# Kernel optimization log

Measured on AMD Instinct MI355X. Metric: run time of the kernel, lower is better.

Reference implementation:

```python
import jax, jax.numpy as jnp
import numpy as np

EMB = 64          # emb_size
LG = 64           # lg_msg_dim
NDB = 16          # num_dist_basis
NCB = 16          # num_cos_basis
NCLS = 40
NLAYERS = 2
NJK = NLAYERS + 2  # jumping-knowledge sequence length
HID = (NJK * EMB) // 2  # PyG JK-LSTM hidden size = 128


def setup_inputs() -> dict:
    key = jax.random.key(0)
    ks = jax.random.split(key, 24)
    N, Eg, Elg, F = 50000, 800000, 800000, 128
    s = 0.05
    inp = {
        "x": jax.random.normal(ks[0], (N, F), jnp.float32),
        "edge_index_g": jax.random.randint(ks[1], (2, Eg), 0, N, jnp.int32),
        "edge_attr_g": jax.random.uniform(ks[2], (Eg, NDB), jnp.float32),
        "edge_index_lg": jax.random.randint(ks[3], (2, Elg), 0, Eg, jnp.int32),
        "edge_attr_lg": jax.random.uniform(ks[4], (Elg, NCB), jnp.float32),
        # parameters (nn.Linear convention: W is [out, in])
        "W_feat": jax.random.normal(ks[5], (EMB, F), jnp.float32) * s,
        "W_msg": jax.random.normal(ks[6], (LG, 2 * EMB + NDB), jnp.float32) * s,
        "W_lg2g": jax.random.normal(ks[7], (EMB, LG), jnp.float32) * s,
        "b_lg2g": jax.random.normal(ks[8], (EMB,), jnp.float32) * s,
        "W_msg_layers": jax.random.normal(ks[9], (NLAYERS, LG, 2 * LG + NCB), jnp.float32) * s,
        # bidirectional LSTM params (PyTorch gate order i,f,g,o)
        "Wih_f": jax.random.normal(ks[10], (4 * HID, EMB), jnp.float32) * s,
        "Whh_f": jax.random.normal(ks[11], (4 * HID, HID), jnp.float32) * s,
        "bih_f": jax.random.normal(ks[12], (4 * HID,), jnp.float32) * s,
        "bhh_f": jax.random.normal(ks[13], (4 * HID,), jnp.float32) * s,
        "Wih_b": jax.random.normal(ks[14], (4 * HID, EMB), jnp.float32) * s,
        "Whh_b": jax.random.normal(ks[15], (4 * HID, HID), jnp.float32) * s,
        "bih_b": jax.random.normal(ks[16], (4 * HID,), jnp.float32) * s,
        "bhh_b": jax.random.normal(ks[17], (4 * HID,), jnp.float32) * s,
        "W_att": jax.random.normal(ks[18], (1, 2 * HID), jnp.float32) * s,
        "b_att": jax.random.normal(ks[19], (1,), jnp.float32) * s,
        "W_out": jax.random.normal(ks[20], (NCLS, EMB), jnp.float32) * s,
    }
    return inp


def _lstm(x_seq, Wih, Whh, bih, bhh, reverse):
    # x_seq: [N, L, C] -> hs: [N, L, H]
    N = x_seq.shape[0]
    H = Whh.shape[1]
    b = bih + bhh

    def step(carry, x_t):
        h, c = carry
        gates = x_t @ Wih.T + h @ Whh.T + b
        i, f, g, o = jnp.split(gates, 4, axis=-1)
        c = jax.nn.sigmoid(f) * c + jax.nn.sigmoid(i) * jnp.tanh(g)
        h = jax.nn.sigmoid(o) * jnp.tanh(c)
        return (h, c), h

    xs = jnp.swapaxes(x_seq, 0, 1)  # [L, N, C]
    init = (jnp.zeros((N, H), x_seq.dtype), jnp.zeros((N, H), x_seq.dtype))
    _, hs = jax.lax.scan(step, init, xs, reverse=reverse)
    return jnp.swapaxes(hs, 0, 1)


def reference(x, edge_index_g, edge_attr_g, edge_index_lg, edge_attr_lg,
              W_feat, W_msg, W_lg2g, b_lg2g, W_msg_layers,
              Wih_f, Whh_f, bih_f, bhh_f, Wih_b, Whh_b, bih_b, bhh_b,
              W_att, b_att, W_out):
    N = x.shape[0]
    Eg = edge_attr_g.shape[0]
    seg = jax.ops.segment_sum

    # node embedding (eval mode: dropout is identity)
    node_emb = jax.nn.relu(x @ W_feat.T)  # [N, EMB]

    # initial linegraph node features: gather endpoints -> concat -> linear -> relu
    m1 = node_emb[edge_index_g[0]]  # [Eg, EMB]
    m2 = node_emb[edge_index_g[1]]
    msg_emb = jax.nn.relu(jnp.concatenate([m1, m2, edge_attr_g], -1) @ W_msg.T)  # [Eg, LG]

    node_embs = [node_emb]
    msg_red = msg_emb @ W_lg2g.T + b_lg2g
    node_embs.append(seg(msg_red, edge_index_g[1], num_segments=N))

    # message-passing layers on the linegraph
    for l in range(W_msg_layers.shape[0]):
        s = msg_emb[edge_index_lg[0]]
        d = msg_emb[edge_index_lg[1]]
        m = jax.nn.relu(jnp.concatenate([s, d, edge_attr_lg], -1) @ W_msg_layers[l].T)
        msg_emb = seg(m, edge_index_lg[1], num_segments=Eg)  # scatter_add over linegraph
        incoming = seg(msg_emb, edge_index_g[1], num_segments=N)
        node_embs.append(incoming @ W_lg2g.T + b_lg2g)

    # JumpingKnowledge ('lstm'): bidirectional LSTM -> attention -> weighted sum
    x_jk = jnp.stack(node_embs, axis=1)  # [N, NJK, EMB]
    h_f = _lstm(x_jk, Wih_f, Whh_f, bih_f, bhh_f, reverse=False)
    h_b = _lstm(x_jk, Wih_b, Whh_b, bih_b, bhh_b, reverse=True)
    h = jnp.concatenate([h_f, h_b], -1)  # [N, NJK, 2*HID]
    alpha = jax.nn.softmax((h @ W_att.T + b_att)[..., 0], axis=-1)  # [N, NJK]
    final_emb = jnp.sum(x_jk * alpha[..., None], axis=1)  # [N, EMB]

    out = final_emb @ W_out.T
    return jax.nn.log_softmax(out, axis=-1)
```

## Files before the change

### kernel.cpp

```cpp
#include <hip/hip_runtime.h>

typedef unsigned short u16;
typedef unsigned int u32;
typedef __attribute__((ext_vector_type(8))) short bf16x8;
typedef __attribute__((ext_vector_type(4))) float f32x4;

#define MFMA(a, b, c) __builtin_amdgcn_mfma_f32_16x16x32_bf16(a, b, c, 0, 0, 0)

__device__ __forceinline__ u16 f2bf(float x) {
    union { float f; u32 u; } v; v.f = x;
    u32 r = (v.u + 0x7FFFu + ((v.u >> 16) & 1u)) >> 16;
    return (u16)r;
}
__device__ __forceinline__ float bf2f(u16 b) {
    union { u32 u; float f; } v; v.u = ((u32)b) << 16;
    return v.f;
}
__device__ __forceinline__ void casAddPair(u32* w, float lo, float hi) {
    u32 old = *w, assumed;
    do {
        assumed = old;
        u32 des = (u32)f2bf(bf2f((u16)(assumed & 0xFFFFu)) + lo) |
                  ((u32)f2bf(bf2f((u16)(assumed >> 16)) + hi) << 16);
        if (des == assumed) break;
        old = atomicCAS(w, assumed, des);
    } while (old != assumed);
}

__global__ __launch_bounds__(256) void prep_w(
    const float* __restrict__ Whh_f, const float* __restrict__ Whh_b,
    const float* __restrict__ Wih_f, const float* __restrict__ Wih_b,
    const float* __restrict__ bih_f, const float* __restrict__ bhh_f,
    const float* __restrict__ bih_b, const float* __restrict__ bhh_b,
    const float* __restrict__ W_feat, const float* __restrict__ W_msg,
    const float* __restrict__ W_msg_l, const float* __restrict__ W_lg2g,
    u16* __restrict__ WhhB, u16* __restrict__ WihB, float* __restrict__ BS,
    u16* __restrict__ WfeatB, u16* __restrict__ WmsgB,
    u16* __restrict__ WmsgLB, u16* __restrict__ Wlg2gB)
{
    const float L2E = 1.4426950408889634f;
    int i = blockIdx.x * 256 + threadIdx.x;
    if (i < 131072) {
        int d = i >> 16, r = i & 65535;
        float s = (((r >> 14) & 3) == 2) ? 2.f * L2E : L2E;
        WhhB[i] = f2bf(s * (d ? Whh_b[r] : Whh_f[r]));
    } else if (i < 196608) {
        int i2 = i - 131072; int d = i2 >> 15, r = i2 & 32767;
        float s = (((r >> 13) & 3) == 2) ? 2.f * L2E : L2E;
        WihB[i2] = f2bf(s * (d ? Wih_b[r] : Wih_f[r]));
    } else if (i < 197632) {
        int i3 = i - 196608; int d = i3 >> 9, g = i3 & 511;
        float s = (((g >> 7) & 3) == 2) ? 2.f * L2E : L2E;
        BS[i3] = s * (d ? (bih_b[g] + bhh_b[g]) : (bih_f[g] + bhh_f[g]));
    } else if (i < 205824) {
        int j = i - 197632; WfeatB[j] = f2bf(W_feat[j]);
    } else if (i < 215040) {
        int j = i - 205824; WmsgB[j] = f2bf(W_msg[j]);
    } else if (i < 233472) {
        int j = i - 215040; WmsgLB[j] = f2bf(W_msg_l[j]);
    } else if (i < 237568) {
        int j = i - 233472; Wlg2gB[j] = f2bf(W_lg2g[j]);
    }
}

__global__ __launch_bounds__(256) void count_kernel(const int* __restrict__ dst,
                                                    u32* __restrict__ cnt, long E)
{
    long i = (long)blockIdx.x * 256 + threadIdx.x;
    if (i < E) atomicAdd(&cnt[dst[i]], 1u);
}

__global__ __launch_bounds__(256) void scan1(const u32* __restrict__ a,
                                             u32* __restrict__ part, int n)
{
    __shared__ u32 ts[256];
    int b = blockIdx.x, t = threadIdx.x;
    long i0 = (long)b * 1024 + t * 4;
    u32 s = 0;
#pragma unroll
    for (int k = 0; k < 4; ++k) { long i = i0 + k; if (i < n) s += a[i]; }
    ts[t] = s; __syncthreads();
    for (int off = 1; off < 256; off <<= 1) {
        u32 x = (t >= off) ? ts[t - off] : 0u;
        __syncthreads(); ts[t] += x; __syncthreads();
    }
    if (t == 255) part[b] = ts[255];
}

__global__ __launch_bounds__(1024) void scan2(u32* __restrict__ part, int nb,
                                              u32* __restrict__ total_out)
{
    __shared__ u32 ts[1024];
    int t = threadIdx.x;
    u32 v = (t < nb) ? part[t] : 0u;
    ts[t] = v; __syncthreads();
    for (int off = 1; off < 1024; off <<= 1) {
        u32 x = (t >= off) ? ts[t - off] : 0u;
        __syncthreads(); ts[t] += x; __syncthreads();
    }
    if (t < nb) part[t] = ts[t] - v;
    if (t == 1023 && total_out) *total_out = ts[1023];
}

__global__ __launch_bounds__(256) void scan3(u32* __restrict__ a,
                                             const u32* __restrict__ part, int n)
{
    __shared__ u32 ts[256];
    int b = blockIdx.x, t = threadIdx.x;
    long i0 = (long)b * 1024 + t * 4;
    u32 v[4]; u32 s = 0;
#pragma unroll
    for (int k = 0; k < 4; ++k) { long i = i0 + k; v[k] = (i < n) ? a[i] : 0u; s += v[k]; }
    ts[t] = s; __syncthreads();
    for (int off = 1; off < 256; off <<= 1) {
        u32 x = (t >= off) ? ts[t - off] : 0u;
        __syncthreads(); ts[t] += x; __syncthreads();
    }
    u32 run = part[b] + ts[t] - s;
#pragma unroll
    for (int k = 0; k < 4; ++k) {
        long i = i0 + k;
        if (i < n) { u32 x = v[k]; a[i] = run; run += x; }
    }
}

__global__ __launch_bounds__(256) void fill_kernel(const int* __restrict__ dst,
                                                   u32* __restrict__ off,
                                                   int* __restrict__ list, long E)
{
    long i = (long)blockIdx.x * 256 + threadIdx.x;
    if (i < E) {
        u32 pos = atomicAdd(&off[dst[i]], 1u);
        list[pos] = (int)i;
    }
}

__global__ __launch_bounds__(256) void zero_fill(const u32* __restrict__ offc,
                                                 u16* __restrict__ outb, long NB)
{
    long idx = (long)blockIdx.x * 256 + threadIdx.x;
    long n = idx >> 3; int q = (int)(idx & 7);
    if (n >= NB) return;
    u32 s = n ? offc[n - 1] : 0u;
    u32 e = offc[n];
    bool need = (s == e) || ((s >> 7) != ((e - 1) >> 7));
    if (need) *(uint4*)(outb + n * 64 + q * 8) = make_uint4(0, 0, 0, 0);
}

template <int K, bool RELU, bool INBF16>
__global__ __launch_bounds__(256) void rowgemm(
    const void* __restrict__ in, const u16* __restrict__ W,
    const float* __restrict__ bias, const float* __restrict__ bias_scale,
    u16* __restrict__ outb, int M)
{
    constexpr int KP = K + 8;
    constexpr int K8 = K / 8;
    __shared__ u16 inS[64 * KP];
    __shared__ u16 WS[64 * KP];
    int t = threadIdx.x;
    long rb = (long)blockIdx.x * 64;
    for (int i = t; i < 64 * K8; i += 256) {
        int c = i / K8, q = i - c * K8;
        *(uint4*)&WS[c * KP + q * 8] = *(const uint4*)&W[c * K + q * 8];
    }
    if (INBF16) {
        const u16* inb = (const u16*)in;
        for (int i = t; i < 64 * K8; i += 256) {
            int r = i / K8, q = i - r * K8;
            long gr = rb + r;
            uint4 v = make_uint4(0, 0, 0, 0);
            if (gr < M) v = *(const uint4*)&inb[gr * (long)K + q * 8];
            *(uint4*)&inS[r * KP + q * 8] = v;
        }
    } else {
        const float* inf = (const float*)in;
        for (int i = t; i < 64 * K; i += 256) {
            int r = i / K, k = i - r * K;
            long gr = rb + r;
            inS[r * KP + k] = (gr < M) ? f2bf(inf[gr * (long)K + k]) : (u16)0;
        }
    }
    __syncthreads();
    int l = t & 63, w = t >> 6, lr = l & 15, lq = l >> 4;
    f32x4 acc[4];
#pragma unroll
    for (int i = 0; i < 4; ++i) acc[i] = (f32x4){0.f, 0.f, 0.f, 0.f};
#pragma unroll
    for (int kc = 0; kc < K; kc += 32) {
        bf16x8 a = *(const bf16x8*)&inS[(w * 16 + lr) * KP + kc + lq * 8];
#pragma unroll
        for (int ct = 0; ct < 4; ++ct) {
            bf16x8 b = *(const bf16x8*)&WS[(ct * 16 + lr) * KP + kc + lq * 8];
            acc[ct] = MFMA(a, b, acc[ct]);
        }
    }
#pragma unroll
    for (int ct = 0; ct < 4; ++ct)
#pragma unroll
        for (int r = 0; r < 4; ++r) {
            long gr = rb + w * 16 + lq * 4 + r;
            if (gr < M) {
                int c = ct * 16 + lr;
                float v = acc[ct][r];
                if (bias) v += bias[c] * (bias_scale ? bias_scale[gr] : 1.f);
                if (RELU) v = fmaxf(v, 0.f);
                outb[gr * 64 + c] = f2bf(v);
            }
        }
}

__global__ __launch_bounds__(512, 4) void edge_msg_init2(
    const u16* __restrict__ feat, const int* __restrict__ ei,
    const float* __restrict__ attr, const u16* __restrict__ W,
    u16* __restrict__ outb, long E)
{
    __shared__ u16 WS[64 * 168];
    __shared__ u16 eds[128 * 64];
    int t = threadIdx.x;
    long eb = (long)blockIdx.x * 128;
    for (int i = t; i < 1152; i += 512) {
        int c = i / 18, q = i - c * 18;
        *(uint4*)&WS[c * 168 + q * 8] = *(const uint4*)&W[c * 144 + q * 8];
    }
    if (t < 192) {
        int c = t / 3, q = t - c * 3;
        *(uint4*)&WS[c * 168 + 144 + q * 8] = make_uint4(0, 0, 0, 0);
    }
    int w = t >> 6, l = t & 63, lr = l & 15, lq = l >> 4;
    long e = eb + w * 16 + lr;
    long ec = (e < E) ? e : (E - 1);
    int src = ei[ec], dst = ei[E + ec];
    bf16x8 A[5];
    {
        const uint4* sp = (const uint4*)(feat + (long)src * 64);
        const uint4* dp = (const uint4*)(feat + (long)dst * 64);
        *(uint4*)&A[0] = sp[lq];
        *(uint4*)&A[1] = sp[4 + lq];
        *(uint4*)&A[2] = dp[lq];
        *(uint4*)&A[3] = dp[4 + lq];
        uint4 pv = make_uint4(0, 0, 0, 0);
        if (lq < 2) {
            const float4* ap = (const float4*)(attr + ec * 16) + lq * 2;
            float4 b0 = ap[0], b1 = ap[1];
            pv.x = (u32)f2bf(b0.x) | ((u32)f2bf(b0.y) << 16);
            pv.y = (u32)f2bf(b0.z) | ((u32)f2bf(b0.w) << 16);
            pv.z = (u32)f2bf(b1.x) | ((u32)f2bf(b1.y) << 16);
            pv.w = (u32)f2bf(b1.z) | ((u32)f2bf(b1.w) << 16);
        }
        *(uint4*)&A[4] = pv;
    }
    __syncthreads();
    f32x4 acc[4];
#pragma unroll
    for (int ct = 0; ct < 4; ++ct) acc[ct] = (f32x4){0.f, 0.f, 0.f, 0.f};
#pragma unroll
    for (int kc = 0; kc < 5; ++kc) {
#pragma unroll
        for (int ct = 0; ct < 4; ++ct) {
            bf16x8 b = *(const bf16x8*)&WS[(ct * 16 + lr) * 168 + kc * 32 + lq * 8];
            acc[ct] = MFMA(A[kc], b, acc[ct]);
        }
    }
#pragma unroll
    for (int ct = 0; ct < 4; ++ct)
#pragma unroll
        for (int r = 0; r < 4; ++r) {
            int row = w * 16 + lq * 4 + r;
            int col = ct * 16 + lr;
            eds[row * 64 + col] = f2bf(fmaxf(acc[ct][r], 0.f));
        }
    __syncthreads();
    for (int j = t; j < 1024; j += 512) {
        int le = j >> 3, q = j & 7;
        long e2 = eb + le;
        if (e2 < E)
            *(uint4*)(outb + e2 * 64 + q * 8) = *(const uint4*)&eds[le * 64 + q * 8];
    }
}

__global__ __launch_bounds__(512, 4) void edge_msg_lg2(
    const u16* __restrict__ feat, const int* __restrict__ ei,
    const float* __restrict__ attr, const u16* __restrict__ W,
    const int* __restrict__ list, u16* __restrict__ outb, long E)
{
    __shared__ u16 WS[64 * 168];
    __shared__ u16 eds[128 * 64];
    __shared__ int dstS[128];
    __shared__ int idS[128];
    __shared__ int srcS[128];
    __shared__ int dprevS, dnextS;
    int t = threadIdx.x;
    long pb = (long)blockIdx.x * 128;
    for (int i = t; i < 1152; i += 512) {
        int c = i / 18, q = i - c * 18;
        *(uint4*)&WS[c * 168 + q * 8] = *(const uint4*)&W[c * 144 + q * 8];
    }
    if (t < 192) {
        int c = t / 3, q = t - c * 3;
        *(uint4*)&WS[c * 168 + 144 + q * 8] = make_uint4(0, 0, 0, 0);
    }
    if (t < 128) {
        long p = pb + t;
        int id = (p < E) ? list[p] : -1;
        idS[t] = id;
        srcS[t] = (id >= 0) ? ei[id] : 0;
        dstS[t] = (id >= 0) ? ei[E + id] : -1;
    } else if (t == 128) {
        dprevS = (pb > 0) ? ei[E + list[pb - 1]] : -2;
    } else if (t == 129) {
        dnextS = (pb + 128 < E) ? ei[E + list[pb + 128]] : -2;
    }
    __syncthreads();
    int w = t >> 6, l = t & 63, lr = l & 15, lq = l >> 4;
    int el = w * 16 + lr;
    int id = idS[el];
    long idc = (id >= 0) ? (long)id : 0;
    int src = srcS[el];
    int dst = (dstS[el] >= 0) ? dstS[el] : 0;
    bf16x8 A[5];
    {
        const uint4* sp = (const uint4*)(feat + (long)src * 64);
        const uint4* dp = (const uint4*)(feat + (long)dst * 64);
        *(uint4*)&A[0] = sp[lq];
        *(uint4*)&A[1] = sp[4 + lq];
        *(uint4*)&A[2] = dp[lq];
        *(uint4*)&A[3] = dp[4 + lq];
        uint4 pv = make_uint4(0, 0, 0, 0);
        if (lq < 2) {
            const float4* ap = (const float4*)(attr + idc * 16) + lq * 2;
            float4 b0 = ap[0], b1 = ap[1];
            pv.x = (u32)f2bf(b0.x) | ((u32)f2bf(b0.y) << 16);
            pv.y = (u32)f2bf(b0.z) | ((u32)f2bf(b0.w) << 16);
            pv.z = (u32)f2bf(b1.x) | ((u32)f2bf(b1.y) << 16);
            pv.w = (u32)f2bf(b1.z) | ((u32)f2bf(b1.w) << 16);
        }
        *(uint4*)&A[4] = pv;
    }
    f32x4 acc[4];
#pragma unroll
    for (int ct = 0; ct < 4; ++ct) acc[ct] = (f32x4){0.f, 0.f, 0.f, 0.f};
#pragma unroll
    for (int kc = 0; kc < 5; ++kc) {
#pragma unroll
        for (int ct = 0; ct < 4; ++ct) {
            bf16x8 b = *(const bf16x8*)&WS[(ct * 16 + lr) * 168 + kc * 32 + lq * 8];
            acc[ct] = MFMA(A[kc], b, acc[ct]);
        }
    }
#pragma unroll
    for (int ct = 0; ct < 4; ++ct)
#pragma unroll
        for (int r = 0; r < 4; ++r) {
            int row = w * 16 + lq * 4 + r;
            int col = ct * 16 + lr;
            eds[row * 64 + col] = f2bf(fmaxf(acc[ct][r], 0.f));
        }
    __syncthreads();
    for (int j = t; j < 4096; j += 512) {
        int le = j >> 5, wd = j & 31;
        int d = dstS[le];
        if (d < 0) continue;
        if (le > 0 && dstS[le - 1] == d) continue;
        float lo = 0.f, hi = 0.f;
        int le2 = le;
        do {
            u32 pair = *(const u32*)&eds[le2 * 64 + wd * 2];
            lo += bf2f((u16)(pair & 0xFFFFu));
            hi += bf2f((u16)(pair >> 16));
            ++le2;
        } while (le2 < 128 && dstS[le2] == d);
        bool bprev = (le == 0 && dprevS == d);
        bool bnext = (le2 == 128 && dnextS == d);
        u32* dw = (u32*)(outb + (long)d * 64 + wd * 2);
        if (bprev || bnext) {
            casAddPair(dw, lo, hi);
        } else {
            *dw = (u32)f2bf(lo) | ((u32)f2bf(hi) << 16);
        }
    }
}

__global__ __launch_bounds__(256) void gather_g(
    const u16* __restrict__ m, const int* __restrict__ list,
    const u32* __restrict__ offc, u16* __restrict__ aggB,
    float* __restrict__ degOut, int N)
{
    int t = threadIdx.x;
    int wv = t >> 6, c = t & 31, half = (t >> 5) & 1;
    long n = (long)blockIdx.x * 4 + wv;
    if (n >= N) return;
    u32 start = n ? offc[n - 1] : 0u;
    u32 end = offc[n];
    float s0 = 0.f, s1 = 0.f;
    for (u32 i = start + half; i < end; i += 2) {
        int e = list[i];
        u32 pair = *(const u32*)&m[(long)e * 64 + c * 2];
        s0 += bf2f((u16)(pair & 0xFFFFu));
        s1 += bf2f((u16)(pair >> 16));
    }
    s0 += __shfl_xor(s0, 32);
    s1 += __shfl_xor(s1, 32);
    if (half == 0)
        *(u32*)&aggB[n * 64 + c * 2] = (u32)f2bf(s0) | ((u32)f2bf(s1) << 16);
    if (degOut && c == 0 && half == 0) degOut[n] = (float)(end - start);
}

__global__ __launch_bounds__(512, 4) void lstm3(
    const u16* __restrict__ jkB, const u16* __restrict__ WhhB,
    const u16* __restrict__ WihB, const float* __restrict__ BS,
    const float* __restrict__ Watt, float* __restrict__ scores,
    int N)
{
    __shared__ u16 hS[64 * 136];
    __shared__ u16 xS[4][64 * 72];
    __shared__ float part[4 * 64 * 8];
    int t = threadIdx.x;
    int dir = blockIdx.y;
    int w = t >> 6, l = t & 63, lr = l & 15, lq = l >> 4;
    const u16* WhhD = WhhB + (long)dir * 65536;
    const u16* WihD = WihB + (long)dir * 32768;
    long n0 = (long)blockIdx.x * 64;

    {
        int n = t >> 3, j = t & 7;
        long gn = n0 + n;
#pragma unroll
        for (int k = 0; k < 4; ++k) {
            uint4 v = make_uint4(0, 0, 0, 0);
            if (gn < N) v = *(const uint4*)&jkB[((long)k * N + gn) * 64 + j * 8];
            *(uint4*)&xS[k][n * 72 + j * 8] = v;
        }
    }

    int grow0 = w * 16 + lq * 4;
    bf16x8 Wh[4][4];
#pragma unroll
    for (int ty = 0; ty < 4; ++ty) {
        int g = ty * 128 + w * 16 + lr;
#pragma unroll
        for (int kc = 0; kc < 4; ++kc)
            Wh[ty][kc] = *(const bf16x8*)&WhhD[g * 128 + kc * 32 + lq * 8];
    }
    const u16* pWiBase = WihD + (w * 16 + lr) * 64 + lq * 8;
    const float* pBBase = BS + dir * 512 + grow0;
    float4 Wa4 = *(const float4*)&Watt[dir * 128 + grow0];
    float* scOut = scores + (long)dir * N * 4;

    float creg[4][4] = {};
    __syncthreads();

#pragma unroll 1
    for (int s = 0; s < 4; ++s) {
        int tt = dir ? (3 - s) : s;
        const u16* pW = pWiBase;
        const float* pBp = pBBase;
        asm volatile("" : "+v"(pW), "+v"(pBp));
        float u[4][4];
        {
            bf16x8 wi0 = *(const bf16x8*)(pW);
            bf16x8 wi1 = *(const bf16x8*)(pW + 32);
            bf16x8 wg0 = *(const bf16x8*)(pW + 16384);
            bf16x8 wg1 = *(const bf16x8*)(pW + 16416);
            f32x4 bi = *(const f32x4*)(pBp);
            f32x4 bg = *(const f32x4*)(pBp + 256);
            f32x4 acc[2][4];
#pragma unroll
            for (int nt = 0; nt < 4; ++nt) {
                acc[0][nt] = (f32x4){0.f, 0.f, 0.f, 0.f};
                acc[1][nt] = (f32x4){0.f, 0.f, 0.f, 0.f};
            }
            if (s) {
#pragma unroll
                for (int kc = 0; kc < 4; ++kc) {
                    bf16x8 a[4];
#pragma unroll
                    for (int nt = 0; nt < 4; ++nt)
                        a[nt] = *(const bf16x8*)&hS[(nt * 16 + lr) * 136 + kc * 32 + lq * 8];
#pragma unroll
                    for (int nt = 0; nt < 4; ++nt) {
                        acc[0][nt] = MFMA(Wh[0][kc], a[nt], acc[0][nt]);
                        acc[1][nt] = MFMA(Wh[2][kc], a[nt], acc[1][nt]);
                    }
                }
            }
#pragma unroll
            for (int kc = 0; kc < 2; ++kc) {
                bf16x8 wi = kc ? wi1 : wi0;
                bf16x8 wg = kc ? wg1 : wg0;
                bf16x8 a[4];
#pragma unroll
                for (int nt = 0; nt < 4; ++nt)
                    a[nt] = *(const bf16x8*)&xS[tt][(nt * 16 + lr) * 72 + kc * 32 + lq * 8];
#pragma unroll
                for (int nt = 0; nt < 4; ++nt) {
                    acc[0][nt] = MFMA(wi, a[nt], acc[0][nt]);
                    acc[1][nt] = MFMA(wg, a[nt], acc[1][nt]);
                }
            }
#pragma unroll
            for (int nt = 0; nt < 4; ++nt)
#pragma unroll
                for (int r = 0; r < 4; ++r) {
                    float si = __builtin_amdgcn_rcpf(
                        1.f + __builtin_amdgcn_exp2f(-(acc[0][nt][r] + bi[r])));
                    float tg = 2.f * __builtin_amdgcn_rcpf(
                        1.f + __builtin_amdgcn_exp2f(-(acc[1][nt][r] + bg[r]))) - 1.f;
                    u[nt][r] = si * tg;
                }
        }
        {
            bf16x8 wf0 = *(const bf16x8*)(pW + 8192);
            bf16x8 wf1 = *(const bf16x8*)(pW + 8224);
            bf16x8 wo0 = *(const bf16x8*)(pW + 24576);
            bf16x8 wo1 = *(const bf16x8*)(pW + 24608);
            f32x4 bfv = *(const f32x4*)(pBp + 128);
            f32x4 bov = *(const f32x4*)(pBp + 384);
            f32x4 acc[2][4];
#pragma unroll
            for (int nt = 0; nt < 4; ++nt) {
                acc[0][nt] = (f32x4){0.f, 0.f, 0.f, 0.f};
                acc[1][nt] = (f32x4){0.f, 0.f, 0.f, 0.f};
            }
            if (s) {
#pragma unroll
                for (int kc = 0; kc < 4; ++kc) {
                    bf16x8 a[4];
#pragma unroll
                    for (int nt = 0; nt < 4; ++nt)
                        a[nt] = *(const bf16x8*)&hS[(nt * 16 + lr) * 136 + kc * 32 + lq * 8];
#pragma unroll
                    for (int nt = 0; nt < 4; ++nt) {
                        acc[0][nt] = MFMA(Wh[1][kc], a[nt], acc[0][nt]);
                        acc[1][nt] = MFMA(Wh[3][kc], a[nt], acc[1][nt]);
                    }
                }
            }
#pragma unroll
            for (int kc = 0; kc < 2; ++kc) {
                bf16x8 wf = kc ? wf1 : wf0;
                bf16x8 wo = kc ? wo1 : wo0;
                bf16x8 a[4];
#pragma unroll
                for (int nt = 0; nt < 4; ++nt)
                    a[nt] = *(const bf16x8*)&xS[tt][(nt * 16 + lr) * 72 + kc * 32 + lq * 8];
#pragma unroll
                for (int nt = 0; nt < 4; ++nt) {
                    acc[0][nt] = MFMA(wf, a[nt], acc[0][nt]);
                    acc[1][nt] = MFMA(wo, a[nt], acc[1][nt]);
                }
            }
            if (s) __syncthreads();
#pragma unroll
            for (int nt = 0; nt < 4; ++nt) {
                float hv[4];
#pragma unroll
                for (int r = 0; r < 4; ++r) {
                    float sf = __builtin_amdgcn_rcpf(
                        1.f + __builtin_amdgcn_exp2f(-(acc[0][nt][r] + bfv[r])));
                    float c = sf * creg[nt][r] + u[nt][r];
                    float so = __builtin_amdgcn_rcpf(
                        1.f + __builtin_amdgcn_exp2f(-(acc[1][nt][r] + bov[r])));
                    float th = 2.f * __builtin_amdgcn_rcpf(
                        1.f + __builtin_amdgcn_exp2f(-2.8853900817779268f * c)) - 1.f;
                    creg[nt][r] = c;
                    hv[r] = so * th;
                }
                float p = hv[0] * Wa4.x + hv[1] * Wa4.y + hv[2] * Wa4.z + hv[3] * Wa4.w;
                p += __shfl_xor(p, 16);
                p += __shfl_xor(p, 32);
                if (lq == 0) part[(tt * 64 + nt * 16 + lr) * 8 + w] = p;
                if (s < 3) {
                    u32 p0, p1;
                    asm("v_cvt_pk_bf16_f32 %0, %1, %2" : "=v"(p0) : "v"(hv[0]), "v"(hv[1]));
                    asm("v_cvt_pk_bf16_f32 %0, %1, %2" : "=v"(p1) : "v"(hv[2]), "v"(hv[3]));
                    *(uint2*)&hS[(nt * 16 + lr) * 136 + grow0] = make_uint2(p0, p1);
                }
            }
        }
        if (s < 3) __syncthreads();
    }
    __syncthreads();
    if (t < 256) {
        int tt = t >> 6, node = t & 63;
        long gn = n0 + node;
        if (gn < N) {
            const float4* pp = (const float4*)&part[(tt * 64 + node) * 8];
            float4 a = pp[0], b = pp[1];
            scOut[gn * 4 + tt] = a.x + a.y + a.z + a.w + b.x + b.y + b.z + b.w;
        }
    }
}

__global__ __launch_bounds__(256) void final_kernel(
    const u16* __restrict__ jkB, const float* __restrict__ scores,
    const float* __restrict__ Wout, float* __restrict__ out, int N)
{
    __shared__ float feS[4][64];
    int t = threadIdx.x, l = t & 63, w = t >> 6;
    long n = (long)blockIdx.x * 4 + w;
    bool ok = (n < N);
    long nn = ok ? n : (long)(N - 1);
    float sc[4];
#pragma unroll
    for (int tt = 0; tt < 4; ++tt)
        sc[tt] = scores[nn * 4 + tt] + scores[(long)N * 4 + nn * 4 + tt];
    float m = fmaxf(fmaxf(sc[0], sc[1]), fmaxf(sc[2], sc[3]));
    float e0 = __expf(sc[0] - m), e1 = __expf(sc[1] - m);
    float e2 = __expf(sc[2] - m), e3 = __expf(sc[3] - m);
    float den = e0 + e1 + e2 + e3;
    float a0 = e0 / den, a1 = e1 / den, a2 = e2 / den, a3 = e3 / den;
    float fe = a0 * bf2f(jkB[nn * 64 + l]) + a1 * bf2f(jkB[((long)N + nn) * 64 + l]) +
               a2 * bf2f(jkB[((long)2 * N + nn) * 64 + l]) +
               a3 * bf2f(jkB[((long)3 * N + nn) * 64 + l]);
    feS[w][l] = fe;
    __syncthreads();
    float logit = 0.f;
    if (l < 40)
        for (int c = 0; c < 64; ++c) logit += feS[w][c] * Wout[l * 64 + c];
    float v = (l < 40) ? logit : -1e30f;
    for (int off = 32; off; off >>= 1) v = fmaxf(v, __shfl_xor(v, off));
    float ex = (l < 40) ? __expf(logit - v) : 0.f;
    for (int off = 32; off; off >>= 1) ex += __shfl_xor(ex, off);
    if (ok && l < 40) out[n * 40 + l] = logit - v - __logf(ex);
}

extern "C" void kernel_launch(void* const* d_in, const int* in_sizes, int n_in,
                              void* d_out, int out_size, void* d_ws, size_t ws_size,
                              hipStream_t stream)
{
    const float* x        = (const float*)d_in[0];
    const int*   eig      = (const int*)d_in[1];
    const float* eag      = (const float*)d_in[2];
    const int*   eilg     = (const int*)d_in[3];
    const float* ealg     = (const float*)d_in[4];
    const float* W_feat   = (const float*)d_in[5];
    const float* W_msg    = (const float*)d_in[6];
    const float* W_lg2g   = (const float*)d_in[7];
    const float* b_lg2g   = (const float*)d_in[8];
    const float* W_msg_l  = (const float*)d_in[9];
    const float* Wih_f    = (const float*)d_in[10];
    const float* Whh_f    = (const float*)d_in[11];
    const float* bih_f    = (const float*)d_in[12];
    const float* bhh_f    = (const float*)d_in[13];
    const float* Wih_b    = (const float*)d_in[14];
    const float* Whh_b    = (const float*)d_in[15];
    const float* bih_b    = (const float*)d_in[16];
    const float* bhh_b    = (const float*)d_in[17];
    const float* W_att    = (const float*)d_in[18];
    const float* W_out    = (const float*)d_in[20];

    int  N   = in_sizes[0] / 128;
    long Eg  = in_sizes[1] / 2;
    long Elg = in_sizes[3] / 2;

    char* wp = (char*)d_ws;
    auto alloc = [&](size_t bytes) -> char* {
        char* p = wp; wp += (bytes + 255) & ~(size_t)255; return p;
    };
    u16*   jkB    = (u16*)  alloc((size_t)4 * N * 64 * 2);
    u16*   mA     = (u16*)  alloc((size_t)Eg * 64 * 2);
    u16*   mB     = (u16*)  alloc((size_t)Eg * 64 * 2);
    u16*   aggB   = (u16*)  alloc((size_t)N * 64 * 2);
    float* deg    = (float*)alloc((size_t)N * 4);
    float* scores = (float*)alloc((size_t)2 * N * 4 * 4);
    u16*   WhhB   = (u16*)  alloc((size_t)2 * 65536 * 2);
    u16*   WihB   = (u16*)  alloc((size_t)2 * 32768 * 2);
    float* BS     = (float*)alloc((size_t)2 * 512 * 4);
    u16*   WfeatB = (u16*)  alloc((size_t)8192 * 2);
    u16*   WmsgB  = (u16*)  alloc((size_t)9216 * 2);
    u16*   WmsgLB = (u16*)  alloc((size_t)18432 * 2);
    u16*   Wlg2gB = (u16*)  alloc((size_t)4096 * 2);
    u32*   off_g  = (u32*)  alloc((size_t)(N + 1) * 4);
    int*   list_g = (int*)  alloc((size_t)Eg * 4);
    u32*   off_lg = (u32*)  alloc((size_t)(Eg + 1) * 4);
    int*   list_lg= (int*)  alloc((size_t)Elg * 4);
    u32*   part   = (u32*)  alloc((size_t)1024 * 4);

    prep_w<<<928, 256, 0, stream>>>(Whh_f, Whh_b, Wih_f, Wih_b,
                                    bih_f, bhh_f, bih_b, bhh_b,
                                    W_feat, W_msg, W_msg_l, W_lg2g,
                                    WhhB, WihB, BS,
                                    WfeatB, WmsgB, WmsgLB, Wlg2gB);
    hipMemsetAsync(off_g, 0, (size_t)(N + 1) * 4, stream);
    count_kernel<<<(int)((Eg + 255) / 256), 256, 0, stream>>>(eig + Eg, off_g, Eg);
    {
        int nb = (N + 1023) / 1024;
        scan1<<<nb, 256, 0, stream>>>(off_g, part, N);
        scan2<<<1, 1024, 0, stream>>>(part, nb, off_g + N);
        scan3<<<nb, 256, 0, stream>>>(off_g, part, N);
    }
    fill_kernel<<<(int)((Eg + 255) / 256), 256, 0, stream>>>(eig + Eg, off_g, list_g, Eg);
    hipMemsetAsync(off_lg, 0, (size_t)(Eg + 1) * 4, stream);
    count_kernel<<<(int)((Elg + 255) / 256), 256, 0, stream>>>(eilg + Elg, off_lg, Elg);
    {
        int nb = (int)((Eg + 1023) / 1024);
        scan1<<<nb, 256, 0, stream>>>(off_lg, part, (int)Eg);
        scan2<<<1, 1024, 0, stream>>>(part, nb, off_lg + Eg);
        scan3<<<nb, 256, 0, stream>>>(off_lg, part, (int)Eg);
    }
    fill_kernel<<<(int)((Elg + 255) / 256), 256, 0, stream>>>(eilg + Elg, off_lg, list_lg, Elg);

    rowgemm<128, true, false><<<(N + 63) / 64, 256, 0, stream>>>(
        x, WfeatB, nullptr, nullptr, jkB, N);
    edge_msg_init2<<<(int)((Eg + 127) / 128), 512, 0, stream>>>(
        jkB, eig, eag, WmsgB, mA, Eg);
    gather_g<<<(N + 3) / 4, 256, 0, stream>>>(mA, list_g, off_g, aggB, deg, N);
    rowgemm<64, false, true><<<(N + 63) / 64, 256, 0, stream>>>(
        aggB, Wlg2gB, b_lg2g, deg, jkB + (size_t)N * 64, N);
    zero_fill<<<(int)((Eg * 8 + 255) / 256), 256, 0, stream>>>(off_lg, mB, Eg);
    edge_msg_lg2<<<(int)((Elg + 127) / 128), 512, 0, stream>>>(
        mA, eilg, ealg, WmsgLB, list_lg, mB, Elg);
    gather_g<<<(N + 3) / 4, 256, 0, stream>>>(mB, list_g, off_g, aggB, nullptr, N);
    rowgemm<64, false, true><<<(N + 63) / 64, 256, 0, stream>>>(
        aggB, Wlg2gB, b_lg2g, nullptr, jkB + (size_t)2 * N * 64, N);
    zero_fill<<<(int)((Eg * 8 + 255) / 256), 256, 0, stream>>>(off_lg, mA, Eg);
    edge_msg_lg2<<<(int)((Elg + 127) / 128), 512, 0, stream>>>(
        mB, eilg, ealg, WmsgLB + 9216, list_lg, mA, Elg);
    gather_g<<<(N + 3) / 4, 256, 0, stream>>>(mA, list_g, off_g, aggB, nullptr, N);
    rowgemm<64, false, true><<<(N + 63) / 64, 256, 0, stream>>>(
        aggB, Wlg2gB, b_lg2g, nullptr, jkB + (size_t)3 * N * 64, N);
    {
        int ntiles = (N + 63) / 64;
        lstm3<<<dim3(ntiles, 2), 512, 0, stream>>>(
            jkB, WhhB, WihB, BS, W_att, scores, N);
    }
    final_kernel<<<(N + 3) / 4, 256, 0, stream>>>(
        jkB, scores, W_out, (float*)d_out, N);
}
```

Measured before the change: 1.185 ms.

## Split LSTM node tiles across 16 waves and stage input weights in LDS

The LSTM kernel now launches 1024 threads per block. The 16 waves are split into two halves, each handling 32 of the 64 nodes, which halves the per-wave MFMA work and accumulator registers. The input-to-hidden weights and biases are copied once into shared memory instead of being reloaded from global memory on every timestep, and the biases are folded into the accumulator initial value. In exchange, each wave still holds the full recurrent weight fragments in registers, LDS use per block grows a lot (about 74 KB more for the input weights), and this may limit how many blocks fit per CU.

```diff
diff --git a/kernel.cpp b/kernel.cpp
--- a/kernel.cpp
+++ b/kernel.cpp
@@ -405,7 +405,7 @@
     if (degOut && c == 0 && half == 0) degOut[n] = (float)(end - start);
 }
 
-__global__ __launch_bounds__(512, 4) void lstm3(
+__global__ __launch_bounds__(1024) void lstm3(
     const u16* __restrict__ jkB, const u16* __restrict__ WhhB,
     const u16* __restrict__ WihB, const float* __restrict__ BS,
     const float* __restrict__ Watt, float* __restrict__ scores,
@@ -413,71 +413,68 @@
 {
     __shared__ u16 hS[64 * 136];
     __shared__ u16 xS[4][64 * 72];
+    __shared__ u16 WiS[512 * 72];
+    __shared__ float bsS[512];
     __shared__ float part[4 * 64 * 8];
     int t = threadIdx.x;
     int dir = blockIdx.y;
     int w = t >> 6, l = t & 63, lr = l & 15, lq = l >> 4;
+    int wl = w & 7, nh = w >> 3;
     const u16* WhhD = WhhB + (long)dir * 65536;
     const u16* WihD = WihB + (long)dir * 32768;
     long n0 = (long)blockIdx.x * 64;
 
-    {
-        int n = t >> 3, j = t & 7;
+#pragma unroll
+    for (int it = 0; it < 2; ++it) {
+        int idx = t + it * 1024;
+        int k = idx >> 9, n = (idx >> 3) & 63, j = idx & 7;
         long gn = n0 + n;
-#pragma unroll
-        for (int k = 0; k < 4; ++k) {
-            uint4 v = make_uint4(0, 0, 0, 0);
-            if (gn < N) v = *(const uint4*)&jkB[((long)k * N + gn) * 64 + j * 8];
-            *(uint4*)&xS[k][n * 72 + j * 8] = v;
-        }
-    }
-
-    int grow0 = w * 16 + lq * 4;
+        uint4 v = make_uint4(0, 0, 0, 0);
+        if (gn < N) v = *(const uint4*)&jkB[((long)k * N + gn) * 64 + j * 8];
+        *(uint4*)&xS[k][n * 72 + j * 8] = v;
+    }
+#pragma unroll
+    for (int it = 0; it < 4; ++it) {
+        int idx = t + it * 1024;
+        int g = idx >> 3, q = idx & 7;
+        *(uint4*)&WiS[g * 72 + q * 8] = *(const uint4*)&WihD[g * 64 + q * 8];
+    }
+    if (t < 512) bsS[t] = BS[dir * 512 + t];
+
+    int grow0 = wl * 16 + lq * 4;
     bf16x8 Wh[4][4];
 #pragma unroll
     for (int ty = 0; ty < 4; ++ty) {
-        int g = ty * 128 + w * 16 + lr;
+        int g = ty * 128 + wl * 16 + lr;
 #pragma unroll
         for (int kc = 0; kc < 4; ++kc)
             Wh[ty][kc] = *(const bf16x8*)&WhhD[g * 128 + kc * 32 + lq * 8];
     }
-    const u16* pWiBase = WihD + (w * 16 + lr) * 64 + lq * 8;
-    const float* pBBase = BS + dir * 512 + grow0;
     float4 Wa4 = *(const float4*)&Watt[dir * 128 + grow0];
     float* scOut = scores + (long)dir * N * 4;
 
-    float creg[4][4] = {};
+    float creg[2][4] = {};
     __syncthreads();
 
 #pragma unroll 1
     for (int s = 0; s < 4; ++s) {
         int tt = dir ? (3 - s) : s;
-        const u16* pW = pWiBase;
-        const float* pBp = pBBase;
-        asm volatile("" : "+v"(pW), "+v"(pBp));
-        float u[4][4];
+        float u[2][4];
         {
-            bf16x8 wi0 = *(const bf16x8*)(pW);
-            bf16x8 wi1 = *(const bf16x8*)(pW + 32);
-            bf16x8 wg0 = *(const bf16x8*)(pW + 16384);
-            bf16x8 wg1 = *(const bf16x8*)(pW + 16416);
-            f32x4 bi = *(const f32x4*)(pBp);
-            f32x4 bg = *(const f32x4*)(pBp + 256);
-            f32x4 acc[2][4];
-#pragma unroll
-            for (int nt = 0; nt < 4; ++nt) {
-                acc[0][nt] = (f32x4){0.f, 0.f, 0.f, 0.f};
-                acc[1][nt] = (f32x4){0.f, 0.f, 0.f, 0.f};
-            }
+            f32x4 acc[2][2];
+            f32x4 bi = *(const f32x4*)&bsS[grow0];
+            f32x4 bg = *(const f32x4*)&bsS[256 + grow0];
+#pragma unroll
+            for (int nt = 0; nt < 2; ++nt) { acc[0][nt] = bi; acc[1][nt] = bg; }
             if (s) {
 #pragma unroll
                 for (int kc = 0; kc < 4; ++kc) {
-                    bf16x8 a[4];
-#pragma unroll
-                    for (int nt = 0; nt < 4; ++nt)
-                        a[nt] = *(const bf16x8*)&hS[(nt * 16 + lr) * 136 + kc * 32 + lq * 8];
-#pragma unroll
-                    for (int nt = 0; nt < 4; ++nt) {
+                    bf16x8 a[2];
+#pragma unroll
+                    for (int nt = 0; nt < 2; ++nt)
+                        a[nt] = *(const bf16x8*)&hS[((nh * 2 + nt) * 16 + lr) * 136 + kc * 32 + lq * 8];
+#pragma unroll
+                    for (int nt = 0; nt < 2; ++nt) {
                         acc[0][nt] = MFMA(Wh[0][kc], a[nt], acc[0][nt]);
                         acc[1][nt] = MFMA(Wh[2][kc], a[nt], acc[1][nt]);
                     }
@@ -485,51 +482,44 @@
             }
 #pragma unroll
             for (int kc = 0; kc < 2; ++kc) {
-                bf16x8 wi = kc ? wi1 : wi0;
-                bf16x8 wg = kc ? wg1 : wg0;
-                bf16x8 a[4];
-#pragma unroll
-                for (int nt = 0; nt < 4; ++nt)
-                    a[nt] = *(const bf16x8*)&xS[tt][(nt * 16 + lr) * 72 + kc * 32 + lq * 8];
-#pragma unroll
-                for (int nt = 0; nt < 4; ++nt) {
+                bf16x8 wi = *(const bf16x8*)&WiS[(wl * 16 + lr) * 72 + kc * 32 + lq * 8];
+                bf16x8 wg = *(const bf16x8*)&WiS[(256 + wl * 16 + lr) * 72 + kc * 32 + lq * 8];
+                bf16x8 a[2];
+#pragma unroll
+                for (int nt = 0; nt < 2; ++nt)
+                    a[nt] = *(const bf16x8*)&xS[tt][((nh * 2 + nt) * 16 + lr) * 72 + kc * 32 + lq * 8];
+#pragma unroll
+                for (int nt = 0; nt < 2; ++nt) {
                     acc[0][nt] = MFMA(wi, a[nt], acc[0][nt]);
                     acc[1][nt] = MFMA(wg, a[nt], acc[1][nt]);
                 }
             }
 #pragma unroll
-            for (int nt = 0; nt < 4; ++nt)
+            for (int nt = 0; nt < 2; ++nt)
 #pragma unroll
                 for (int r = 0; r < 4; ++r) {
                     float si = __builtin_amdgcn_rcpf(
-                        1.f + __builtin_amdgcn_exp2f(-(acc[0][nt][r] + bi[r])));
+                        1.f + __builtin_amdgcn_exp2f(-acc[0][nt][r]));
                     float tg = 2.f * __builtin_amdgcn_rcpf(
-                        1.f + __builtin_amdgcn_exp2f(-(acc[1][nt][r] + bg[r]))) - 1.f;
+                        1.f + __builtin_amdgcn_exp2f(-acc[1][nt][r])) - 1.f;
                     u[nt][r] = si * tg;
                 }
         }
         {
-            bf16x8 wf0 = *(const bf16x8*)(pW + 8192);
-            bf16x8 wf1 = *(const bf16x8*)(pW + 8224);
-            bf16x8 wo0 = *(const bf16x8*)(pW + 24576);
-            bf16x8 wo1 = *(const bf16x8*)(pW + 24608);
-            f32x4 bfv = *(const f32x4*)(pBp + 128);
-            f32x4 bov = *(const f32x4*)(pBp + 384);
-            f32x4 acc[2][4];
-#pragma unroll
-            for (int nt = 0; nt < 4; ++nt) {
-                acc[0][nt] = (f32x4){0.f, 0.f, 0.f, 0.f};
-                acc[1][nt] = (f32x4){0.f, 0.f, 0.f, 0.f};
-            }
+            f32x4 acc[2][2];
+            f32x4 bf = *(const f32x4*)&bsS[128 + grow0];
+            f32x4 bo = *(const f32x4*)&bsS[384 + grow0];
+#pragma unroll
+            for (int nt = 0; nt < 2; ++nt) { acc[0][nt] = bf; acc[1][nt] = bo; }
             if (s) {
 #pragma unroll
                 for (int kc = 0; kc < 4; ++kc) {
-                    bf16x8 a[4];
-#pragma unroll
-                    for (int nt = 0; nt < 4; ++nt)
-                        a[nt] = *(const bf16x8*)&hS[(nt * 16 + lr) * 136 + kc * 32 + lq * 8];
-#pragma unroll
-                    for (int nt = 0; nt < 4; ++nt) {
+                    bf16x8 a[2];
+#pragma unroll
+                    for (int nt = 0; nt < 2; ++nt)
+                        a[nt] = *(const bf16x8*)&hS[((nh * 2 + nt) * 16 + lr) * 136 + kc * 32 + lq * 8];
+#pragma unroll
+                    for (int nt = 0; nt < 2; ++nt) {
                         acc[0][nt] = MFMA(Wh[1][kc], a[nt], acc[0][nt]);
                         acc[1][nt] = MFMA(Wh[3][kc], a[nt], acc[1][nt]);
                     }
@@ -537,43 +527,44 @@
             }
 #pragma unroll
             for (int kc = 0; kc < 2; ++kc) {
-                bf16x8 wf = kc ? wf1 : wf0;
-                bf16x8 wo = kc ? wo1 : wo0;
-                bf16x8 a[4];
-#pragma unroll
-                for (int nt = 0; nt < 4; ++nt)
-                    a[nt] = *(const bf16x8*)&xS[tt][(nt * 16 + lr) * 72 + kc * 32 + lq * 8];
-#pragma unroll
-                for (int nt = 0; nt < 4; ++nt) {
+                bf16x8 wf = *(const bf16x8*)&WiS[(128 + wl * 16 + lr) * 72 + kc * 32 + lq * 8];
+                bf16x8 wo = *(const bf16x8*)&WiS[(384 + wl * 16 + lr) * 72 + kc * 32 + lq * 8];
+                bf16x8 a[2];
+#pragma unroll
+                for (int nt = 0; nt < 2; ++nt)
+                    a[nt] = *(const bf16x8*)&xS[tt][((nh * 2 + nt) * 16 + lr) * 72 + kc * 32 + lq * 8];
+#pragma unroll
+                for (int nt = 0; nt < 2; ++nt) {
                     acc[0][nt] = MFMA(wf, a[nt], acc[0][nt]);
                     acc[1][nt] = MFMA(wo, a[nt], acc[1][nt]);
                 }
             }
             if (s) __syncthreads();
 #pragma unroll
-            for (int nt = 0; nt < 4; ++nt) {
+            for (int nt = 0; nt < 2; ++nt) {
                 float hv[4];
 #pragma unroll
                 for (int r = 0; r < 4; ++r) {
                     float sf = __builtin_amdgcn_rcpf(
-                        1.f + __builtin_amdgcn_exp2f(-(acc[0][nt][r] + bfv[r])));
+                        1.f + __builtin_amdgcn_exp2f(-acc[0][nt][r]));
                     float c = sf * creg[nt][r] + u[nt][r];
                     float so = __builtin_amdgcn_rcpf(
-                        1.f + __builtin_amdgcn_exp2f(-(acc[1][nt][r] + bov[r])));
+                        1.f + __builtin_amdgcn_exp2f(-acc[1][nt][r]));
                     float th = 2.f * __builtin_amdgcn_rcpf(
                         1.f + __builtin_amdgcn_exp2f(-2.8853900817779268f * c)) - 1.f;
                     creg[nt][r] = c;
                     hv[r] = so * th;
                 }
+                int node = (nh * 2 + nt) * 16 + lr;
                 float p = hv[0] * Wa4.x + hv[1] * Wa4.y + hv[2] * Wa4.z + hv[3] * Wa4.w;
                 p += __shfl_xor(p, 16);
                 p += __shfl_xor(p, 32);
-                if (lq == 0) part[(tt * 64 + nt * 16 + lr) * 8 + w] = p;
+                if (lq == 0) part[(tt * 64 + node) * 8 + wl] = p;
                 if (s < 3) {
                     u32 p0, p1;
                     asm("v_cvt_pk_bf16_f32 %0, %1, %2" : "=v"(p0) : "v"(hv[0]), "v"(hv[1]));
                     asm("v_cvt_pk_bf16_f32 %0, %1, %2" : "=v"(p1) : "v"(hv[2]), "v"(hv[3]));
-                    *(uint2*)&hS[(nt * 16 + lr) * 136 + grow0] = make_uint2(p0, p1);
+                    *(uint2*)&hS[node * 136 + grow0] = make_uint2(p0, p1);
                 }
             }
         }
@@ -721,7 +712,7 @@
         aggB, Wlg2gB, b_lg2g, nullptr, jkB + (size_t)3 * N * 64, N);
     {
         int ntiles = (N + 63) / 64;
-        lstm3<<<dim3(ntiles, 2), 512, 0, stream>>>(
+        lstm3<<<dim3(ntiles, 2), 1024, 0, stream>>>(
             jkB, WhhB, WihB, BS, W_att, scores, N);
     }
     final_kernel<<<(N + 3) / 4, 256, 0, stream>>>(
```

New measurement: 1.074 ms. -9.4%, faster.
